# Kernel tuning notes

Hardware: AMD Instinct MI355X
Metric: run time of the kernel (lower is better)

The kernel has to match this reference:

```python
import jax, jax.numpy as jnp
import numpy as np

N_NODES = 50000
N_EDGES = 1600000
ATOM_F = 64
FP_SIZE = 2048
N_GRAPHS = 2000


def setup_inputs() -> dict:
    key = jax.random.key(0)
    ks = jax.random.split(key, 12)
    s = 1.0 / np.sqrt(ATOM_F)
    x = jax.random.normal(ks[0], (N_NODES, ATOM_F), dtype=jnp.float32)
    H1_w = jax.random.normal(ks[1], (ATOM_F, ATOM_F), dtype=jnp.float32) * s
    H1_b = jnp.zeros((ATOM_F,), dtype=jnp.float32)
    W1_w = jax.random.normal(ks[2], (FP_SIZE, ATOM_F), dtype=jnp.float32) * s
    W1_b = jnp.zeros((FP_SIZE,), dtype=jnp.float32)
    H2_w = jax.random.normal(ks[3], (ATOM_F, ATOM_F), dtype=jnp.float32) * s
    H2_b = jnp.zeros((ATOM_F,), dtype=jnp.float32)
    W2_w = jax.random.normal(ks[4], (FP_SIZE, ATOM_F), dtype=jnp.float32) * s
    W2_b = jnp.zeros((FP_SIZE,), dtype=jnp.float32)
    edge_index = jax.random.randint(ks[5], (2, N_EDGES), 0, N_NODES, dtype=jnp.int64)
    batch = jnp.sort(jax.random.randint(ks[6], (N_NODES,), 0, N_GRAPHS, dtype=jnp.int64))
    return {
        "x": x,
        "H1_w": H1_w, "H1_b": H1_b, "W1_w": W1_w, "W1_b": W1_b,
        "H2_w": H2_w, "H2_b": H2_b, "W2_w": W2_w, "W2_b": W2_b,
        "edge_index": edge_index,
        "batch": batch,
        "num_graphs": N_GRAPHS,
    }


def reference(x, H1_w, H1_b, W1_w, W1_b, H2_w, H2_b, W2_w, W2_b,
              edge_index, batch, num_graphs):
    n = x.shape[0]
    src, dst = edge_index[0], edge_index[1]

    def loop(h, Hw, Hb, Ww, Wb):
        # sum aggregation over incoming edges; '+ h' accounts for add_self_loops
        agg = jax.ops.segment_sum(h[src], dst, num_segments=n) + h
        upd = jax.nn.sigmoid(agg @ Hw.T + Hb)          # [N, atom_features]
        fp = jax.nn.softmax(upd @ Ww.T + Wb, axis=-1)  # [N, fp_size]
        return upd, fp

    h1, fp1 = loop(x, H1_w, H1_b, W1_w, W1_b)
    _, fp2 = loop(h1, H2_w, H2_b, W2_w, W2_b)
    fingerprint = fp1 + fp2
    # pool per-node fingerprints into per-graph fingerprints
    return jax.ops.segment_sum(fingerprint, batch, num_segments=num_graphs)
```

## Files before the change

### kernel.cpp

```cpp
#include <hip/hip_runtime.h>
#include <hip/hip_bf16.h>

#define AF 64
#define NFP 2048
#define MAXG 3
#define LOG2E 1.4426950408889634f

typedef __attribute__((ext_vector_type(8))) short bf16x8;
typedef __attribute__((ext_vector_type(4))) float f32x4;

__device__ __forceinline__ ushort f2bf(float f) {
    unsigned u = __float_as_uint(f);
    return (ushort)((u + 0x7FFF + ((u >> 16) & 1)) >> 16);
}
__device__ __forceinline__ float bf2f(ushort u) {
    return __uint_as_float((unsigned)u << 16);
}

__global__ __launch_bounds__(256) void hist_kernel(
    const int* __restrict__ keys, int* __restrict__ counts, int n)
{
    int e = blockIdx.x * 256 + threadIdx.x;
    if (e < n) atomicAdd(&counts[keys[e]], 1);
}

__global__ __launch_bounds__(256) void hist_part_kernel(
    const int* __restrict__ dst, int* __restrict__ counts,
    int n_edges, int npr, int nchunks)
{
    int r = blockIdx.x & 7;
    int c = blockIdx.x >> 3;
    int lo = r * npr, hi = lo + npr;
    int per = (n_edges + nchunks - 1) / nchunks;
    int e0 = c * per;
    int e1 = e0 + per; if (e1 > n_edges) e1 = n_edges;
    for (int e = e0 + (int)threadIdx.x; e < e1; e += 256) {
        int d = dst[e];
        if (d >= lo && d < hi) atomicAdd(&counts[d], 1);
    }
}

__global__ __launch_bounds__(1024) void scan_kernel(int* data, int n)
{
    __shared__ int wsum[16];
    __shared__ int chunk_total;
    int t = threadIdx.x, lane = t & 63, w = t >> 6;
    int running = 0;
    for (int base = 0; base < n; base += 1024) {
        int i = base + t;
        int v = (i < n) ? data[i] : 0;
        int x = v;
        #pragma unroll
        for (int off = 1; off < 64; off <<= 1) {
            int y = __shfl_up(x, off);
            if (lane >= off) x += y;
        }
        if (lane == 63) wsum[w] = x;
        __syncthreads();
        if (t == 0) {
            int s = 0;
            #pragma unroll
            for (int q = 0; q < 16; ++q) { int tmp = wsum[q]; wsum[q] = s; s += tmp; }
            chunk_total = s;
        }
        __syncthreads();
        if (i < n) data[i] = x - v + wsum[w] + running;
        running += chunk_total;
        __syncthreads();
    }
    if (t == 0) data[n] = running;
}

__global__ __launch_bounds__(1024) void scan_block_kernel(
    int* __restrict__ data, int* __restrict__ bsum, int n)
{
    __shared__ int wsum[16];
    int t = threadIdx.x, lane = t & 63, w = t >> 6;
    int i = blockIdx.x * 1024 + t;
    int v = (i < n) ? data[i] : 0;
    int x = v;
    #pragma unroll
    for (int off = 1; off < 64; off <<= 1) {
        int y = __shfl_up(x, off);
        if (lane >= off) x += y;
    }
    if (lane == 63) wsum[w] = x;
    __syncthreads();
    if (t == 0) {
        int s = 0;
        #pragma unroll
        for (int q = 0; q < 16; ++q) { int tmp = wsum[q]; wsum[q] = s; s += tmp; }
        bsum[blockIdx.x] = s;
    }
    __syncthreads();
    if (i < n) data[i] = x - v + wsum[w];
}

__global__ __launch_bounds__(1024) void scan_sums_kernel(int* bsum, int nb)
{
    __shared__ int wsum[16];
    int t = threadIdx.x, lane = t & 63, w = t >> 6;
    int v = (t < nb) ? bsum[t] : 0;
    int x = v;
    #pragma unroll
    for (int off = 1; off < 64; off <<= 1) {
        int y = __shfl_up(x, off);
        if (lane >= off) x += y;
    }
    if (lane == 63) wsum[w] = x;
    __syncthreads();
    if (t == 0) {
        int s = 0;
        #pragma unroll
        for (int q = 0; q < 16; ++q) { int tmp = wsum[q]; wsum[q] = s; s += tmp; }
        bsum[nb] = s;
    }
    __syncthreads();
    if (t < nb) bsum[t] = x - v + wsum[w];
}

__global__ __launch_bounds__(256) void scan_add_kernel(
    int* __restrict__ data, const int* __restrict__ bsum, int n, int nb)
{
    int i = blockIdx.x * 256 + threadIdx.x;
    if (i < n) data[i] += bsum[i >> 10];
    if (i == 0) data[n] = bsum[nb];
}

__global__ __launch_bounds__(256) void scatter_part_kernel(
    const int* __restrict__ src, const int* __restrict__ dst,
    int* __restrict__ cursor, int* __restrict__ esrc,
    int n_edges, int npr, int nchunks)
{
    int r = blockIdx.x & 7;
    int c = blockIdx.x >> 3;
    int lo = r * npr, hi = lo + npr;
    int per = (n_edges + nchunks - 1) / nchunks;
    int e0 = c * per;
    int e1 = e0 + per; if (e1 > n_edges) e1 = n_edges;
    for (int e = e0 + (int)threadIdx.x; e < e1; e += 256) {
        int d = dst[e];
        if (d >= lo && d < hi) {
            int pos = atomicAdd(&cursor[d], 1);
            esrc[pos] = src[e];
        }
    }
}

__global__ __launch_bounds__(256) void f2bf_kernel(
    const float* __restrict__ W, ushort* __restrict__ Wbf, float scale, int n)
{
    int i = blockIdx.x * 256 + threadIdx.x;
    if (i < n) Wbf[i] = f2bf(W[i] * scale);
}

__global__ __launch_bounds__(256) void agg_mlp_kernel(
    const ushort* __restrict__ hbf, const int* __restrict__ offsets,
    const int* __restrict__ esrc, const float* __restrict__ Hw,
    const float* __restrict__ Hb, ushort* __restrict__ outbf, int n_nodes)
{
    __shared__ float Hw_s[AF * 65];
    __shared__ __align__(16) float part[4][8][AF];
    __shared__ float a_red[4][AF];
    __shared__ float hb_s[AF];

    int t = threadIdx.x;
    for (int idx = t; idx < AF * AF; idx += 256) {
        int j = idx >> 6, k = idx & 63;
        Hw_s[j * 65 + k] = Hw[idx];
    }
    if (t < AF) hb_s[t] = Hb[t];

    int w = t >> 6, lane = t & 63;
    int sub = lane >> 3, f8 = lane & 7;
    int i = blockIdx.x * 4 + w;

    float acc[8] = {0.f, 0.f, 0.f, 0.f, 0.f, 0.f, 0.f, 0.f};
    if (i < n_nodes) {
        int o0 = offsets[i], o1 = offsets[i + 1];
        const int* ep = esrc + o0;
        int deg = o1 - o0;
        for (int j = 0; j < deg; j += 8) {
            int jj = j + sub;
            if (jj < deg) {
                int s = ep[jj];
                bf16x8 v = *(const bf16x8*)(hbf + (size_t)s * AF + f8 * 8);
                #pragma unroll
                for (int q = 0; q < 8; ++q) acc[q] += bf2f((ushort)v[q]);
            }
        }
    }
    *(float4*)&part[w][sub][f8 * 8]     = make_float4(acc[0], acc[1], acc[2], acc[3]);
    *(float4*)&part[w][sub][f8 * 8 + 4] = make_float4(acc[4], acc[5], acc[6], acc[7]);
    __syncthreads();

    if (i < n_nodes) {
        float val = bf2f(hbf[(size_t)i * AF + lane]);
        #pragma unroll
        for (int s8 = 0; s8 < 8; ++s8) val += part[w][s8][lane];
        a_red[w][lane] = val;
    }
    __syncthreads();

    if (i < n_nodes) {
        float z = hb_s[lane];
        #pragma unroll
        for (int k = 0; k < AF; ++k)
            z = fmaf(a_red[w][k], Hw_s[lane * 65 + k], z);
        float sg = 1.f / (1.f + __expf(-z));
        outbf[(size_t)i * AF + lane] = f2bf(sg);
    }
}

__global__ __launch_bounds__(256) void fp_node_pool_kernel(
    const ushort* __restrict__ updbf, const ushort* __restrict__ Wbf,
    const float* __restrict__ Wb, const int* __restrict__ batch,
    float* __restrict__ partial, float* __restrict__ out, int n_nodes)
{
    __shared__ float red[4][32];
    __shared__ float sden_s[32];
    __shared__ int   bat_s[32];
    __shared__ float wb_s[NFP];
    __shared__ __align__(16) float pacc[MAXG][NFP];

    int t = threadIdx.x, wave = t >> 6, lane = t & 63;
    int G = lane >> 4, sl = lane & 15;
    int cw = wave * 512;
    int b = blockIdx.x;
    int i0 = b * 32;

    #pragma unroll
    for (int j = 0; j < NFP / 256; ++j)
        wb_s[j * 256 + t] = Wb[j * 256 + t] * LOG2E;
    if (t < 32) {
        int n = i0 + t;
        bat_s[t] = batch[n < n_nodes ? n : (n_nodes - 1)];
    }

    bf16x8 a00, a01, a10, a11;
    {
        const ushort* p0 = updbf + (size_t)(i0 + sl) * AF + G * 8;
        a00 = *(const bf16x8*)p0;
        a01 = *(const bf16x8*)(p0 + 32);
        const ushort* p1 = updbf + (size_t)(i0 + 16 + sl) * AF + G * 8;
        a10 = *(const bf16x8*)p1;
        a11 = *(const bf16x8*)(p1 + 32);
    }
    __syncthreads();

    float s0[4] = {0.f, 0.f, 0.f, 0.f};
    float s1[4] = {0.f, 0.f, 0.f, 0.f};
    {
        const ushort* wp0 = Wbf + (size_t)(cw + sl) * AF + G * 8;
        bf16x8 nb0 = *(const bf16x8*)wp0;
        bf16x8 nb1 = *(const bf16x8*)(wp0 + 32);
        #pragma unroll 4
        for (int ct = 0; ct < 32; ++ct) {
            bf16x8 b0 = nb0, b1 = nb1;
            if (ct < 31) {
                const ushort* wp = Wbf + (size_t)(cw + (ct + 1) * 16 + sl) * AF + G * 8;
                nb0 = *(const bf16x8*)wp;
                nb1 = *(const bf16x8*)(wp + 32);
            }
            float bias = wb_s[cw + ct * 16 + sl];
            f32x4 d0 = {0.f, 0.f, 0.f, 0.f};
            d0 = __builtin_amdgcn_mfma_f32_16x16x32_bf16(a00, b0, d0, 0, 0, 0);
            d0 = __builtin_amdgcn_mfma_f32_16x16x32_bf16(a01, b1, d0, 0, 0, 0);
            f32x4 d1 = {0.f, 0.f, 0.f, 0.f};
            d1 = __builtin_amdgcn_mfma_f32_16x16x32_bf16(a10, b0, d1, 0, 0, 0);
            d1 = __builtin_amdgcn_mfma_f32_16x16x32_bf16(a11, b1, d1, 0, 0, 0);
            #pragma unroll
            for (int r = 0; r < 4; ++r) {
                s0[r] += __builtin_amdgcn_exp2f(d0[r] + bias);
                s1[r] += __builtin_amdgcn_exp2f(d1[r] + bias);
            }
        }
    }
    #pragma unroll
    for (int mask = 1; mask <= 8; mask <<= 1) {
        #pragma unroll
        for (int r = 0; r < 4; ++r) {
            s0[r] += __shfl_xor(s0[r], mask);
            s1[r] += __shfl_xor(s1[r], mask);
        }
    }
    if (sl == 0) {
        #pragma unroll
        for (int r = 0; r < 4; ++r) {
            red[wave][G * 4 + r]      = s0[r];
            red[wave][16 + G * 4 + r] = s1[r];
        }
    }
    __syncthreads();
    if (t < 32) {
        float s = red[0][t] + red[1][t] + red[2][t] + red[3][t];
        sden_s[t] = 1.f / s;
    }
    __syncthreads();

    int g_first = bat_s[0];
    int ng = bat_s[31] - g_first + 1;
    int ngl = ng < MAXG ? ng : MAXG;

    for (int gi = 0; gi < ngl; ++gi) {
        *(float4*)&pacc[gi][cw + lane * 8]     = make_float4(0.f, 0.f, 0.f, 0.f);
        *(float4*)&pacc[gi][cw + lane * 8 + 4] = make_float4(0.f, 0.f, 0.f, 0.f);
    }

    float sc0[4], sc1[4];
    int gl0[4], gl1[4];
    #pragma unroll
    for (int r = 0; r < 4; ++r) {
        int l0 = G * 4 + r, l1 = l0 + 16;
        sc0[r] = (i0 + l0 < n_nodes) ? sden_s[l0] : 0.f;
        sc1[r] = (i0 + l1 < n_nodes) ? sden_s[l1] : 0.f;
        gl0[r] = bat_s[l0];
        gl1[r] = bat_s[l1];
    }

    {
        const ushort* wp0 = Wbf + (size_t)(cw + sl) * AF + G * 8;
        bf16x8 nb0 = *(const bf16x8*)wp0;
        bf16x8 nb1 = *(const bf16x8*)(wp0 + 32);
        #pragma unroll 4
        for (int ct = 0; ct < 32; ++ct) {
            bf16x8 b0 = nb0, b1 = nb1;
            if (ct < 31) {
                const ushort* wp = Wbf + (size_t)(cw + (ct + 1) * 16 + sl) * AF + G * 8;
                nb0 = *(const bf16x8*)wp;
                nb1 = *(const bf16x8*)(wp + 32);
            }
            int col = cw + ct * 16 + sl;
            float bias = wb_s[col];
            f32x4 d0 = {0.f, 0.f, 0.f, 0.f};
            d0 = __builtin_amdgcn_mfma_f32_16x16x32_bf16(a00, b0, d0, 0, 0, 0);
            d0 = __builtin_amdgcn_mfma_f32_16x16x32_bf16(a01, b1, d0, 0, 0, 0);
            f32x4 d1 = {0.f, 0.f, 0.f, 0.f};
            d1 = __builtin_amdgcn_mfma_f32_16x16x32_bf16(a10, b0, d1, 0, 0, 0);
            d1 = __builtin_amdgcn_mfma_f32_16x16x32_bf16(a11, b1, d1, 0, 0, 0);
            float e0[4], e1[4];
            #pragma unroll
            for (int r = 0; r < 4; ++r) {
                e0[r] = __builtin_amdgcn_exp2f(d0[r] + bias) * sc0[r];
                e1[r] = __builtin_amdgcn_exp2f(d1[r] + bias) * sc1[r];
            }
            for (int gi = 0; gi < ng; ++gi) {
                int g = g_first + gi;
                float c = 0.f;
                #pragma unroll
                for (int r = 0; r < 4; ++r) {
                    c += (gl0[r] == g) ? e0[r] : 0.f;
                    c += (gl1[r] == g) ? e1[r] : 0.f;
                }
                c += __shfl_xor(c, 16);
                c += __shfl_xor(c, 32);
                if (gi < MAXG) {
                    if (G == 0) pacc[gi][col] += c;
                } else if (G == 0) {
                    unsafeAtomicAdd(&out[(size_t)g * NFP + col], c);
                }
            }
        }
    }

    for (int gi = 0; gi < ng; ++gi) {
        float* row = partial + (size_t)(b + g_first + gi) * NFP;
        if (gi < MAXG) {
            *(float4*)&row[cw + lane * 8]     = *(float4*)&pacc[gi][cw + lane * 8];
            *(float4*)&row[cw + lane * 8 + 4] = *(float4*)&pacc[gi][cw + lane * 8 + 4];
        } else {
            *(float4*)&row[cw + lane * 8]     = make_float4(0.f, 0.f, 0.f, 0.f);
            *(float4*)&row[cw + lane * 8 + 4] = make_float4(0.f, 0.f, 0.f, 0.f);
        }
    }
}

__global__ __launch_bounds__(256) void fp_reduce_kernel(
    const float* __restrict__ partial, const int* __restrict__ goff,
    float* __restrict__ out)
{
    int g = blockIdx.x, t = threadIdx.x;
    int gs = goff[g], ge = goff[g + 1];
    if (ge <= gs) return;
    int b0 = gs >> 5, b1 = (ge - 1) >> 5;
    float4 acc0 = make_float4(0.f, 0.f, 0.f, 0.f);
    float4 acc1 = make_float4(0.f, 0.f, 0.f, 0.f);
    for (int b = b0; b <= b1; ++b) {
        const float* row = partial + (size_t)(b + g) * NFP;
        float4 v0 = *(const float4*)&row[t * 8];
        float4 v1 = *(const float4*)&row[t * 8 + 4];
        acc0.x += v0.x; acc0.y += v0.y; acc0.z += v0.z; acc0.w += v0.w;
        acc1.x += v1.x; acc1.y += v1.y; acc1.z += v1.z; acc1.w += v1.w;
    }
    float* po = &out[(size_t)g * NFP];
    float4 o0 = *(float4*)&po[t * 8];
    float4 o1 = *(float4*)&po[t * 8 + 4];
    o0.x += acc0.x; o0.y += acc0.y; o0.z += acc0.z; o0.w += acc0.w;
    o1.x += acc1.x; o1.y += acc1.y; o1.z += acc1.z; o1.w += acc1.w;
    *(float4*)&po[t * 8]     = o0;
    *(float4*)&po[t * 8 + 4] = o1;
}

extern "C" void kernel_launch(void* const* d_in, const int* in_sizes, int n_in,
                              void* d_out, int out_size, void* d_ws, size_t ws_size,
                              hipStream_t stream)
{
    const float* x    = (const float*)d_in[0];
    const float* H1_w = (const float*)d_in[1];
    const float* H1_b = (const float*)d_in[2];
    const float* W1_w = (const float*)d_in[3];
    const float* W1_b = (const float*)d_in[4];
    const float* H2_w = (const float*)d_in[5];
    const float* H2_b = (const float*)d_in[6];
    const float* W2_w = (const float*)d_in[7];
    const float* W2_b = (const float*)d_in[8];
    const int*   ei   = (const int*)d_in[9];
    const int*   batch= (const int*)d_in[10];

    const int n_nodes  = in_sizes[0] / AF;
    const int n_edges  = in_sizes[9] / 2;
    const int n_graphs = out_size / NFP;
    const int npad     = ((n_nodes + 127) / 128) * 128;
    const int* src = ei;
    const int* dst = ei + n_edges;
    float* out = (float*)d_out;

    const int fp_blocks = (n_nodes + 31) / 32;
    const int npairs    = fp_blocks + n_graphs + 1;
    const int nsb       = (n_nodes + 1023) / 1024;

    ushort* xbf     = (ushort*)d_ws;
    ushort* ubf1    = xbf  + (size_t)npad * AF;
    ushort* ubf2    = ubf1 + (size_t)npad * AF;
    ushort* Wbf1    = ubf2 + (size_t)npad * AF;
    ushort* Wbf2    = Wbf1 + (size_t)NFP * AF;
    float*  partial = (float*)(Wbf2 + (size_t)NFP * AF);
    int*    offsets = (int*)(partial + (size_t)npairs * NFP);
    int*    cursor  = offsets + (n_nodes + 1);
    int*    goff    = cursor + (n_nodes + 1);
    int*    bscan   = goff + (n_graphs + 1);
    int*    esrc    = bscan + (nsb + 1);

    const int nb = (n_nodes + 255) / 256;
    const int mlp_blocks = (n_nodes + 3) / 4;
    const int wn = NFP * AF;
    const int xn = n_nodes * AF;
    const int npr = (n_nodes + 7) / 8;
    const int nchunks = 256;

    f2bf_kernel<<<(xn + 255) / 256, 256, 0, stream>>>(x, xbf, 1.0f, xn);
    f2bf_kernel<<<(wn + 255) / 256, 256, 0, stream>>>(W1_w, Wbf1, LOG2E, wn);
    f2bf_kernel<<<(wn + 255) / 256, 256, 0, stream>>>(W2_w, Wbf2, LOG2E, wn);
    hipMemsetAsync(out, 0, (size_t)out_size * sizeof(float), stream);
    hipMemsetAsync(xbf + (size_t)n_nodes * AF, 0,
                   (size_t)(npad - n_nodes) * AF * sizeof(ushort), stream);
    hipMemsetAsync(ubf1 + (size_t)n_nodes * AF, 0,
                   (size_t)(npad - n_nodes) * AF * sizeof(ushort), stream);
    hipMemsetAsync(ubf2 + (size_t)n_nodes * AF, 0,
                   (size_t)(npad - n_nodes) * AF * sizeof(ushort), stream);
    hipMemsetAsync(offsets, 0, (size_t)(n_nodes + 1) * sizeof(int), stream);
    hipMemsetAsync(goff, 0, (size_t)(n_graphs + 1) * sizeof(int), stream);
    hist_part_kernel<<<nchunks * 8, 256, 0, stream>>>(dst, offsets, n_edges, npr, nchunks);
    hist_kernel<<<nb, 256, 0, stream>>>(batch, goff, n_nodes);
    scan_block_kernel<<<nsb, 1024, 0, stream>>>(offsets, bscan, n_nodes);
    scan_sums_kernel<<<1, 1024, 0, stream>>>(bscan, nsb);
    scan_add_kernel<<<(n_nodes + 255) / 256, 256, 0, stream>>>(offsets, bscan,
                                                               n_nodes, nsb);
    scan_kernel<<<1, 1024, 0, stream>>>(goff, n_graphs);
    hipMemcpyAsync(cursor, offsets, (size_t)n_nodes * sizeof(int),
                   hipMemcpyDeviceToDevice, stream);
    scatter_part_kernel<<<nchunks * 8, 256, 0, stream>>>(src, dst, cursor, esrc,
                                                         n_edges, npr, nchunks);

    agg_mlp_kernel<<<mlp_blocks, 256, 0, stream>>>(xbf, offsets, esrc,
                                                   H1_w, H1_b, ubf1, n_nodes);
    fp_node_pool_kernel<<<fp_blocks, 256, 0, stream>>>(ubf1, Wbf1, W1_b, batch,
                                                       partial, out, n_nodes);
    fp_reduce_kernel<<<n_graphs, 256, 0, stream>>>(partial, goff, out);

    agg_mlp_kernel<<<mlp_blocks, 256, 0, stream>>>(ubf1, offsets, esrc,
                                                   H2_w, H2_b, ubf2, n_nodes);
    fp_node_pool_kernel<<<fp_blocks, 256, 0, stream>>>(ubf2, Wbf2, W2_b, batch,
                                                       partial, out, n_nodes);
    fp_reduce_kernel<<<n_graphs, 256, 0, stream>>>(partial, goff, out);
}
```

Before: 595.2 us.

## Fuse layer-1 fingerprint pooling with layer-2 aggregation; cache exps in second FP kernel

```diff
diff --git a/kernel.cpp b/kernel.cpp
--- a/kernel.cpp
+++ b/kernel.cpp
@@ -212,177 +212,372 @@
     }
 }
 
-__global__ __launch_bounds__(256) void fp_node_pool_kernel(
+__global__ __launch_bounds__(256) void fused_fp1_agg2_kernel(
+    const ushort* __restrict__ ubf1, const ushort* __restrict__ Wbf1,
+    const float* __restrict__ W1b, const int* __restrict__ batch,
+    float* __restrict__ partial, float* __restrict__ out,
+    const int* __restrict__ offsets, const int* __restrict__ esrc,
+    const float* __restrict__ H2w, const float* __restrict__ H2b,
+    ushort* __restrict__ ubf2, int n_nodes, int fpb)
+{
+    __shared__ __align__(16) char smem[33536];
+    int t = threadIdx.x;
+
+    if ((int)blockIdx.x < fpb) {
+        float* wb_s   = (float*)smem;
+        float (*pacc)[NFP] = (float(*)[NFP])(smem + 8192);
+        float (*red)[32]   = (float(*)[32])(smem + 32768);
+        float* sden_s = (float*)(smem + 33280);
+        int*   bat_s  = (int*)(smem + 33408);
+
+        int wave = t >> 6, lane = t & 63;
+        int G = lane >> 4, sl = lane & 15;
+        int cw = wave * 512;
+        int b = blockIdx.x;
+        int i0 = b * 32;
+
+        #pragma unroll
+        for (int j = 0; j < NFP / 256; ++j)
+            wb_s[j * 256 + t] = W1b[j * 256 + t] * LOG2E;
+        if (t < 32) {
+            int n = i0 + t;
+            bat_s[t] = batch[n < n_nodes ? n : (n_nodes - 1)];
+        }
+
+        bf16x8 a00, a01, a10, a11;
+        {
+            const ushort* p0 = ubf1 + (size_t)(i0 + sl) * AF + G * 8;
+            a00 = *(const bf16x8*)p0;
+            a01 = *(const bf16x8*)(p0 + 32);
+            const ushort* p1 = ubf1 + (size_t)(i0 + 16 + sl) * AF + G * 8;
+            a10 = *(const bf16x8*)p1;
+            a11 = *(const bf16x8*)(p1 + 32);
+        }
+        __syncthreads();
+
+        float s0[4] = {0.f, 0.f, 0.f, 0.f};
+        float s1[4] = {0.f, 0.f, 0.f, 0.f};
+        {
+            const ushort* wp0 = Wbf1 + (size_t)(cw + sl) * AF + G * 8;
+            bf16x8 nb0 = *(const bf16x8*)wp0;
+            bf16x8 nb1 = *(const bf16x8*)(wp0 + 32);
+            #pragma unroll 4
+            for (int ct = 0; ct < 32; ++ct) {
+                bf16x8 b0 = nb0, b1 = nb1;
+                if (ct < 31) {
+                    const ushort* wp = Wbf1 + (size_t)(cw + (ct + 1) * 16 + sl) * AF + G * 8;
+                    nb0 = *(const bf16x8*)wp;
+                    nb1 = *(const bf16x8*)(wp + 32);
+                }
+                float bias = wb_s[cw + ct * 16 + sl];
+                f32x4 d0 = {0.f, 0.f, 0.f, 0.f};
+                d0 = __builtin_amdgcn_mfma_f32_16x16x32_bf16(a00, b0, d0, 0, 0, 0);
+                d0 = __builtin_amdgcn_mfma_f32_16x16x32_bf16(a01, b1, d0, 0, 0, 0);
+                f32x4 d1 = {0.f, 0.f, 0.f, 0.f};
+                d1 = __builtin_amdgcn_mfma_f32_16x16x32_bf16(a10, b0, d1, 0, 0, 0);
+                d1 = __builtin_amdgcn_mfma_f32_16x16x32_bf16(a11, b1, d1, 0, 0, 0);
+                #pragma unroll
+                for (int r = 0; r < 4; ++r) {
+                    s0[r] += __builtin_amdgcn_exp2f(d0[r] + bias);
+                    s1[r] += __builtin_amdgcn_exp2f(d1[r] + bias);
+                }
+            }
+        }
+        #pragma unroll
+        for (int mask = 1; mask <= 8; mask <<= 1) {
+            #pragma unroll
+            for (int r = 0; r < 4; ++r) {
+                s0[r] += __shfl_xor(s0[r], mask);
+                s1[r] += __shfl_xor(s1[r], mask);
+            }
+        }
+        if (sl == 0) {
+            #pragma unroll
+            for (int r = 0; r < 4; ++r) {
+                red[wave][G * 4 + r]      = s0[r];
+                red[wave][16 + G * 4 + r] = s1[r];
+            }
+        }
+        __syncthreads();
+        if (t < 32) {
+            float s = red[0][t] + red[1][t] + red[2][t] + red[3][t];
+            sden_s[t] = 1.f / s;
+        }
+        __syncthreads();
+
+        int g_first = bat_s[0];
+        int ng = bat_s[31] - g_first + 1;
+        int ngl = ng < MAXG ? ng : MAXG;
+
+        for (int gi = 0; gi < ngl; ++gi) {
+            *(float4*)&pacc[gi][cw + lane * 8]     = make_float4(0.f, 0.f, 0.f, 0.f);
+            *(float4*)&pacc[gi][cw + lane * 8 + 4] = make_float4(0.f, 0.f, 0.f, 0.f);
+        }
+
+        float sc0[4], sc1[4];
+        int gl0[4], gl1[4];
+        #pragma unroll
+        for (int r = 0; r < 4; ++r) {
+            int l0 = G * 4 + r, l1 = l0 + 16;
+            sc0[r] = (i0 + l0 < n_nodes) ? sden_s[l0] : 0.f;
+            sc1[r] = (i0 + l1 < n_nodes) ? sden_s[l1] : 0.f;
+            gl0[r] = bat_s[l0];
+            gl1[r] = bat_s[l1];
+        }
+
+        {
+            const ushort* wp0 = Wbf1 + (size_t)(cw + sl) * AF + G * 8;
+            bf16x8 nb0 = *(const bf16x8*)wp0;
+            bf16x8 nb1 = *(const bf16x8*)(wp0 + 32);
+            #pragma unroll 4
+            for (int ct = 0; ct < 32; ++ct) {
+                bf16x8 b0 = nb0, b1 = nb1;
+                if (ct < 31) {
+                    const ushort* wp = Wbf1 + (size_t)(cw + (ct + 1) * 16 + sl) * AF + G * 8;
+                    nb0 = *(const bf16x8*)wp;
+                    nb1 = *(const bf16x8*)(wp + 32);
+                }
+                int col = cw + ct * 16 + sl;
+                float bias = wb_s[col];
+                f32x4 d0 = {0.f, 0.f, 0.f, 0.f};
+                d0 = __builtin_amdgcn_mfma_f32_16x16x32_bf16(a00, b0, d0, 0, 0, 0);
+                d0 = __builtin_amdgcn_mfma_f32_16x16x32_bf16(a01, b1, d0, 0, 0, 0);
+                f32x4 d1 = {0.f, 0.f, 0.f, 0.f};
+                d1 = __builtin_amdgcn_mfma_f32_16x16x32_bf16(a10, b0, d1, 0, 0, 0);
+                d1 = __builtin_amdgcn_mfma_f32_16x16x32_bf16(a11, b1, d1, 0, 0, 0);
+                float e0[4], e1[4];
+                #pragma unroll
+                for (int r = 0; r < 4; ++r) {
+                    e0[r] = __builtin_amdgcn_exp2f(d0[r] + bias) * sc0[r];
+                    e1[r] = __builtin_amdgcn_exp2f(d1[r] + bias) * sc1[r];
+                }
+                for (int gi = 0; gi < ng; ++gi) {
+                    int g = g_first + gi;
+                    float c = 0.f;
+                    #pragma unroll
+                    for (int r = 0; r < 4; ++r) {
+                        c += (gl0[r] == g) ? e0[r] : 0.f;
+                        c += (gl1[r] == g) ? e1[r] : 0.f;
+                    }
+                    c += __shfl_xor(c, 16);
+                    c += __shfl_xor(c, 32);
+                    if (gi < MAXG) {
+                        if (G == 0) pacc[gi][col] += c;
+                    } else if (G == 0) {
+                        unsafeAtomicAdd(&out[(size_t)g * NFP + col], c);
+                    }
+                }
+            }
+        }
+
+        for (int gi = 0; gi < ng; ++gi) {
+            float* row = partial + (size_t)(b + g_first + gi) * NFP;
+            if (gi < MAXG) {
+                *(float4*)&row[cw + lane * 8]     = *(float4*)&pacc[gi][cw + lane * 8];
+                *(float4*)&row[cw + lane * 8 + 4] = *(float4*)&pacc[gi][cw + lane * 8 + 4];
+            } else {
+                *(float4*)&row[cw + lane * 8]     = make_float4(0.f, 0.f, 0.f, 0.f);
+                *(float4*)&row[cw + lane * 8 + 4] = make_float4(0.f, 0.f, 0.f, 0.f);
+            }
+        }
+    } else {
+        float* Hw_s = (float*)smem;
+        float (*part)[8][AF] = (float(*)[8][AF])(smem + 16640);
+        float (*a_red)[AF]   = (float(*)[AF])(smem + 24832);
+        float* hb_s = (float*)(smem + 25856);
+
+        for (int idx = t; idx < AF * AF; idx += 256) {
+            int j = idx >> 6, k = idx & 63;
+            Hw_s[j * 65 + k] = H2w[idx];
+        }
+        if (t < AF) hb_s[t] = H2b[t];
+
+        int w = t >> 6, lane = t & 63;
+        int sub = lane >> 3, f8 = lane & 7;
+        int i = (blockIdx.x - fpb) * 4 + w;
+
+        float acc[8] = {0.f, 0.f, 0.f, 0.f, 0.f, 0.f, 0.f, 0.f};
+        if (i < n_nodes) {
+            int o0 = offsets[i], o1 = offsets[i + 1];
+            const int* ep = esrc + o0;
+            int deg = o1 - o0;
+            for (int j = 0; j < deg; j += 8) {
+                int jj = j + sub;
+                if (jj < deg) {
+                    int s = ep[jj];
+                    bf16x8 v = *(const bf16x8*)(ubf1 + (size_t)s * AF + f8 * 8);
+                    #pragma unroll
+                    for (int q = 0; q < 8; ++q) acc[q] += bf2f((ushort)v[q]);
+                }
+            }
+        }
+        *(float4*)&part[w][sub][f8 * 8]     = make_float4(acc[0], acc[1], acc[2], acc[3]);
+        *(float4*)&part[w][sub][f8 * 8 + 4] = make_float4(acc[4], acc[5], acc[6], acc[7]);
+        __syncthreads();
+
+        if (i < n_nodes) {
+            float val = bf2f(ubf1[(size_t)i * AF + lane]);
+            #pragma unroll
+            for (int s8 = 0; s8 < 8; ++s8) val += part[w][s8][lane];
+            a_red[w][lane] = val;
+        }
+        __syncthreads();
+
+        if (i < n_nodes) {
+            float z = hb_s[lane];
+            #pragma unroll
+            for (int k = 0; k < AF; ++k)
+                z = fmaf(a_red[w][k], Hw_s[lane * 65 + k], z);
+            float sg = 1.f / (1.f + __expf(-z));
+            ubf2[(size_t)i * AF + lane] = f2bf(sg);
+        }
+    }
+}
+
+__global__ __launch_bounds__(512) void fp_node_pool_kernel(
     const ushort* __restrict__ updbf, const ushort* __restrict__ Wbf,
     const float* __restrict__ Wb, const int* __restrict__ batch,
     float* __restrict__ partial, float* __restrict__ out, int n_nodes)
 {
-    __shared__ float red[4][32];
-    __shared__ float sden_s[32];
-    __shared__ int   bat_s[32];
+    __shared__ float red[8][16];
+    __shared__ float sden_s[16];
+    __shared__ int   bat_s[16];
     __shared__ float wb_s[NFP];
     __shared__ __align__(16) float pacc[MAXG][NFP];
 
     int t = threadIdx.x, wave = t >> 6, lane = t & 63;
     int G = lane >> 4, sl = lane & 15;
-    int cw = wave * 512;
+    int cw = wave * 256;
     int b = blockIdx.x;
-    int i0 = b * 32;
+    int i0 = b * 16;
 
     #pragma unroll
-    for (int j = 0; j < NFP / 256; ++j)
-        wb_s[j * 256 + t] = Wb[j * 256 + t] * LOG2E;
-    if (t < 32) {
+    for (int j = 0; j < NFP / 512; ++j)
+        wb_s[j * 512 + t] = Wb[j * 512 + t] * LOG2E;
+    if (t < 16) {
         int n = i0 + t;
         bat_s[t] = batch[n < n_nodes ? n : (n_nodes - 1)];
     }
 
-    bf16x8 a00, a01, a10, a11;
+    bf16x8 a0, a1;
     {
         const ushort* p0 = updbf + (size_t)(i0 + sl) * AF + G * 8;
-        a00 = *(const bf16x8*)p0;
-        a01 = *(const bf16x8*)(p0 + 32);
-        const ushort* p1 = updbf + (size_t)(i0 + 16 + sl) * AF + G * 8;
-        a10 = *(const bf16x8*)p1;
-        a11 = *(const bf16x8*)(p1 + 32);
+        a0 = *(const bf16x8*)p0;
+        a1 = *(const bf16x8*)(p0 + 32);
     }
     __syncthreads();
 
     float s0[4] = {0.f, 0.f, 0.f, 0.f};
-    float s1[4] = {0.f, 0.f, 0.f, 0.f};
+    float ef[16][4];
     {
         const ushort* wp0 = Wbf + (size_t)(cw + sl) * AF + G * 8;
         bf16x8 nb0 = *(const bf16x8*)wp0;
         bf16x8 nb1 = *(const bf16x8*)(wp0 + 32);
-        #pragma unroll 4
-        for (int ct = 0; ct < 32; ++ct) {
+        #pragma unroll
+        for (int ct = 0; ct < 16; ++ct) {
             bf16x8 b0 = nb0, b1 = nb1;
-            if (ct < 31) {
+            if (ct < 15) {
                 const ushort* wp = Wbf + (size_t)(cw + (ct + 1) * 16 + sl) * AF + G * 8;
                 nb0 = *(const bf16x8*)wp;
                 nb1 = *(const bf16x8*)(wp + 32);
             }
             float bias = wb_s[cw + ct * 16 + sl];
-            f32x4 d0 = {0.f, 0.f, 0.f, 0.f};
-            d0 = __builtin_amdgcn_mfma_f32_16x16x32_bf16(a00, b0, d0, 0, 0, 0);
-            d0 = __builtin_amdgcn_mfma_f32_16x16x32_bf16(a01, b1, d0, 0, 0, 0);
-            f32x4 d1 = {0.f, 0.f, 0.f, 0.f};
-            d1 = __builtin_amdgcn_mfma_f32_16x16x32_bf16(a10, b0, d1, 0, 0, 0);
-            d1 = __builtin_amdgcn_mfma_f32_16x16x32_bf16(a11, b1, d1, 0, 0, 0);
+            f32x4 d = {0.f, 0.f, 0.f, 0.f};
+            d = __builtin_amdgcn_mfma_f32_16x16x32_bf16(a0, b0, d, 0, 0, 0);
+            d = __builtin_amdgcn_mfma_f32_16x16x32_bf16(a1, b1, d, 0, 0, 0);
             #pragma unroll
             for (int r = 0; r < 4; ++r) {
-                s0[r] += __builtin_amdgcn_exp2f(d0[r] + bias);
-                s1[r] += __builtin_amdgcn_exp2f(d1[r] + bias);
+                float e = __builtin_amdgcn_exp2f(d[r] + bias);
+                ef[ct][r] = e;
+                s0[r] += e;
             }
         }
     }
     #pragma unroll
     for (int mask = 1; mask <= 8; mask <<= 1) {
         #pragma unroll
-        for (int r = 0; r < 4; ++r) {
-            s0[r] += __shfl_xor(s0[r], mask);
-            s1[r] += __shfl_xor(s1[r], mask);
-        }
+        for (int r = 0; r < 4; ++r) s0[r] += __shfl_xor(s0[r], mask);
     }
     if (sl == 0) {
         #pragma unroll
-        for (int r = 0; r < 4; ++r) {
-            red[wave][G * 4 + r]      = s0[r];
-            red[wave][16 + G * 4 + r] = s1[r];
-        }
-    }
-    __syncthreads();
-    if (t < 32) {
-        float s = red[0][t] + red[1][t] + red[2][t] + red[3][t];
+        for (int r = 0; r < 4; ++r) red[wave][G * 4 + r] = s0[r];
+    }
+    __syncthreads();
+    if (t < 16) {
+        float s = 0.f;
+        #pragma unroll
+        for (int w8 = 0; w8 < 8; ++w8) s += red[w8][t];
         sden_s[t] = 1.f / s;
     }
     __syncthreads();
 
     int g_first = bat_s[0];
-    int ng = bat_s[31] - g_first + 1;
+    int ng = bat_s[15] - g_first + 1;
     int ngl = ng < MAXG ? ng : MAXG;
 
-    for (int gi = 0; gi < ngl; ++gi) {
-        *(float4*)&pacc[gi][cw + lane * 8]     = make_float4(0.f, 0.f, 0.f, 0.f);
-        *(float4*)&pacc[gi][cw + lane * 8 + 4] = make_float4(0.f, 0.f, 0.f, 0.f);
-    }
-
-    float sc0[4], sc1[4];
-    int gl0[4], gl1[4];
+    for (int gi = 0; gi < ngl; ++gi)
+        *(float4*)&pacc[gi][cw + lane * 4] = make_float4(0.f, 0.f, 0.f, 0.f);
+
+    float sc0[4];
+    int gl0[4];
     #pragma unroll
     for (int r = 0; r < 4; ++r) {
-        int l0 = G * 4 + r, l1 = l0 + 16;
+        int l0 = G * 4 + r;
         sc0[r] = (i0 + l0 < n_nodes) ? sden_s[l0] : 0.f;
-        sc1[r] = (i0 + l1 < n_nodes) ? sden_s[l1] : 0.f;
         gl0[r] = bat_s[l0];
-        gl1[r] = bat_s[l1];
-    }
-
-    {
-        const ushort* wp0 = Wbf + (size_t)(cw + sl) * AF + G * 8;
-        bf16x8 nb0 = *(const bf16x8*)wp0;
-        bf16x8 nb1 = *(const bf16x8*)(wp0 + 32);
-        #pragma unroll 4
-        for (int ct = 0; ct < 32; ++ct) {
-            bf16x8 b0 = nb0, b1 = nb1;
-            if (ct < 31) {
-                const ushort* wp = Wbf + (size_t)(cw + (ct + 1) * 16 + sl) * AF + G * 8;
-                nb0 = *(const bf16x8*)wp;
-                nb1 = *(const bf16x8*)(wp + 32);
-            }
-            int col = cw + ct * 16 + sl;
-            float bias = wb_s[col];
-            f32x4 d0 = {0.f, 0.f, 0.f, 0.f};
-            d0 = __builtin_amdgcn_mfma_f32_16x16x32_bf16(a00, b0, d0, 0, 0, 0);
-            d0 = __builtin_amdgcn_mfma_f32_16x16x32_bf16(a01, b1, d0, 0, 0, 0);
-            f32x4 d1 = {0.f, 0.f, 0.f, 0.f};
-            d1 = __builtin_amdgcn_mfma_f32_16x16x32_bf16(a10, b0, d1, 0, 0, 0);
-            d1 = __builtin_amdgcn_mfma_f32_16x16x32_bf16(a11, b1, d1, 0, 0, 0);
-            float e0[4], e1[4];
-            #pragma unroll
-            for (int r = 0; r < 4; ++r) {
-                e0[r] = __builtin_amdgcn_exp2f(d0[r] + bias) * sc0[r];
-                e1[r] = __builtin_amdgcn_exp2f(d1[r] + bias) * sc1[r];
-            }
-            for (int gi = 0; gi < ng; ++gi) {
-                int g = g_first + gi;
-                float c = 0.f;
-                #pragma unroll
-                for (int r = 0; r < 4; ++r) {
-                    c += (gl0[r] == g) ? e0[r] : 0.f;
-                    c += (gl1[r] == g) ? e1[r] : 0.f;
-                }
+    }
+    #pragma unroll
+    for (int ct = 0; ct < 16; ++ct) {
+        #pragma unroll
+        for (int r = 0; r < 4; ++r) ef[ct][r] *= sc0[r];
+    }
+
+    for (int gi = 0; gi < ng; ++gi) {
+        int g = g_first + gi;
+        if (gi < MAXG) {
+            #pragma unroll
+            for (int ct = 0; ct < 16; ++ct) {
+                int col = cw + ct * 16 + sl;
+                float c = ((gl0[0] == g) ? ef[ct][0] : 0.f)
+                        + ((gl0[1] == g) ? ef[ct][1] : 0.f)
+                        + ((gl0[2] == g) ? ef[ct][2] : 0.f)
+                        + ((gl0[3] == g) ? ef[ct][3] : 0.f);
                 c += __shfl_xor(c, 16);
                 c += __shfl_xor(c, 32);
-                if (gi < MAXG) {
-                    if (G == 0) pacc[gi][col] += c;
-                } else if (G == 0) {
+                if (G == 0) pacc[gi][col] += c;
+            }
+        } else {
+            #pragma unroll
+            for (int ct = 0; ct < 16; ++ct) {
+                int col = cw + ct * 16 + sl;
+                float c = ((gl0[0] == g) ? ef[ct][0] : 0.f)
+                        + ((gl0[1] == g) ? ef[ct][1] : 0.f)
+                        + ((gl0[2] == g) ? ef[ct][2] : 0.f)
+                        + ((gl0[3] == g) ? ef[ct][3] : 0.f);
+                c += __shfl_xor(c, 16);
+                c += __shfl_xor(c, 32);
+                if (G == 0)
                     unsafeAtomicAdd(&out[(size_t)g * NFP + col], c);
-                }
             }
         }
     }
 
     for (int gi = 0; gi < ng; ++gi) {
         float* row = partial + (size_t)(b + g_first + gi) * NFP;
-        if (gi < MAXG) {
-            *(float4*)&row[cw + lane * 8]     = *(float4*)&pacc[gi][cw + lane * 8];
-            *(float4*)&row[cw + lane * 8 + 4] = *(float4*)&pacc[gi][cw + lane * 8 + 4];
-        } else {
-            *(float4*)&row[cw + lane * 8]     = make_float4(0.f, 0.f, 0.f, 0.f);
-            *(float4*)&row[cw + lane * 8 + 4] = make_float4(0.f, 0.f, 0.f, 0.f);
-        }
+        float4 v = make_float4(0.f, 0.f, 0.f, 0.f);
+        if (gi < MAXG) v = *(float4*)&pacc[gi][cw + lane * 4];
+        *(float4*)&row[cw + lane * 4] = v;
     }
 }
 
 __global__ __launch_bounds__(256) void fp_reduce_kernel(
     const float* __restrict__ partial, const int* __restrict__ goff,
-    float* __restrict__ out)
+    float* __restrict__ out, int shift)
 {
     int g = blockIdx.x, t = threadIdx.x;
     int gs = goff[g], ge = goff[g + 1];
     if (ge <= gs) return;
-    int b0 = gs >> 5, b1 = (ge - 1) >> 5;
+    int b0 = gs >> shift, b1 = (ge - 1) >> shift;
     float4 acc0 = make_float4(0.f, 0.f, 0.f, 0.f);
     float4 acc1 = make_float4(0.f, 0.f, 0.f, 0.f);
     for (int b = b0; b <= b1; ++b) {
@@ -425,9 +620,10 @@
     const int* dst = ei + n_edges;
     float* out = (float*)d_out;
 
-    const int fp_blocks = (n_nodes + 31) / 32;
-    const int npairs    = fp_blocks + n_graphs + 1;
-    const int nsb       = (n_nodes + 1023) / 1024;
+    const int fpb32 = (n_nodes + 31) / 32;
+    const int fpb16 = (n_nodes + 15) / 16;
+    const int npairs = fpb16 + n_graphs + 1;
+    const int nsb    = (n_nodes + 1023) / 1024;
 
     ushort* xbf     = (ushort*)d_ws;
     ushort* ubf1    = xbf  + (size_t)npad * AF;
@@ -474,13 +670,13 @@
 
     agg_mlp_kernel<<<mlp_blocks, 256, 0, stream>>>(xbf, offsets, esrc,
                                                    H1_w, H1_b, ubf1, n_nodes);
-    fp_node_pool_kernel<<<fp_blocks, 256, 0, stream>>>(ubf1, Wbf1, W1_b, batch,
-                                                       partial, out, n_nodes);
-    fp_reduce_kernel<<<n_graphs, 256, 0, stream>>>(partial, goff, out);
-
-    agg_mlp_kernel<<<mlp_blocks, 256, 0, stream>>>(ubf1, offsets, esrc,
-                                                   H2_w, H2_b, ubf2, n_nodes);
-    fp_node_pool_kernel<<<fp_blocks, 256, 0, stream>>>(ubf2, Wbf2, W2_b, batch,
-                                                       partial, out, n_nodes);
-    fp_reduce_kernel<<<n_graphs, 256, 0, stream>>>(partial, goff, out);
-}
+
+    fused_fp1_agg2_kernel<<<fpb32 + mlp_blocks, 256, 0, stream>>>(
+        ubf1, Wbf1, W1_b, batch, partial, out,
+        offsets, esrc, H2_w, H2_b, ubf2, n_nodes, fpb32);
+    fp_reduce_kernel<<<n_graphs, 256, 0, stream>>>(partial, goff, out, 5);
+
+    fp_node_pool_kernel<<<fpb16, 512, 0, stream>>>(ubf2, Wbf2, W2_b, batch,
+                                                   partial, out, n_nodes);
+    fp_reduce_kernel<<<n_graphs, 256, 0, stream>>>(partial, goff, out, 4);
+}
```

Result: no change. 587.5 us (-1.3%).
